# Optimization experiments

Measured on AMD Instinct MI355X. Metric: run time of the kernel, lower is better.

## Reference

```python
import jax, jax.numpy as jnp
import numpy as np

# dims: batch, seq, model, heads, head_dim, mlp, layers, vocab, window
B, S, D, H, DH, M, L, V, W = 2, 2048, 512, 8, 64, 2048, 6, 32000, 512
EPS = 1e-6
NEG = -1e9

def _sinusoidal(max_len, d):
    # LRA common_layers sinusoidal_init (min_scale=1, max_scale=1e4)
    pe = np.zeros((max_len, d), np.float32)
    position = np.arange(max_len)[:, None].astype(np.float32)
    scale_factor = -np.log(1e4) / (d // 2 - 1)
    div_term = np.exp(np.arange(d // 2).astype(np.float32) * scale_factor)
    pe[:, : d // 2] = np.sin(position * div_term)
    pe[:, d // 2 :] = np.cos(position * div_term)
    return jnp.asarray(pe)[None]  # [1, S, D]

POS_EMB = _sinusoidal(S, D)

def _ln(x, scale, bias):
    mu = jnp.mean(x, -1, keepdims=True)
    var = jnp.mean(jnp.square(x - mu), -1, keepdims=True)
    return (x - mu) * jax.lax.rsqrt(var + EPS) * scale + bias

def setup_inputs() -> dict:
    key = jax.random.key(0)
    ks = jax.random.split(key, 16)
    def n(k, shape, s=0.02):
        return jax.random.normal(k, shape, jnp.float32) * s
    return {
        "inputs": jax.random.randint(ks[0], (B, S), 0, V),
        "emb": n(ks[1], (V, D), 1.0),          # nn.Embed normal(stddev=1)
        "wq": n(ks[2], (L, D, H, DH)),
        "wk": n(ks[3], (L, D, H, DH)),
        "wv": n(ks[4], (L, D, H, DH)),
        "wo": n(ks[5], (L, H, DH, D)),
        "ln1_s": 1.0 + n(ks[6], (L, D)),
        "ln1_b": n(ks[7], (L, D)),
        "ln2_s": 1.0 + n(ks[8], (L, D)),
        "ln2_b": n(ks[9], (L, D)),
        "w1": n(ks[10], (L, D, M)),
        "b1": n(ks[11], (L, M), 1e-6),
        "w2": n(ks[12], (L, M, D)),
        "b2": n(ks[13], (L, D), 1e-6),
        "lnf_s": 1.0 + n(ks[14], (D,)),
        "lnf_b": n(ks[15], (D,)),
    }

def reference(inputs, emb, wq, wk, wv, wo, ln1_s, ln1_b, ln2_s, ln2_b,
              w1, b1, w2, b2, lnf_s, lnf_b):
    pad = inputs > 0                                  # [B,S] padding mask
    x = emb[inputs] + POS_EMB                         # embed + sinusoidal pos
    idx = jnp.arange(S)
    band = jnp.abs(idx[:, None] - idx[None, :]) <= (W // 2)  # sliding window
    mask = band[None, None] & pad[:, None, :, None] & pad[:, None, None, :]
    attn_bias = jnp.where(mask, 0.0, NEG)             # [B,1,S,S]
    scale = 1.0 / jnp.sqrt(jnp.float32(DH))
    for l in range(L):
        # --- Longformer self-attention (pre-LN) ---
        y = _ln(x, ln1_s[l], ln1_b[l])
        q = jnp.einsum('bsd,dhk->bshk', y, wq[l]) * scale
        k = jnp.einsum('bsd,dhk->bshk', y, wk[l])
        v = jnp.einsum('bsd,dhk->bshk', y, wv[l])
        logits = jnp.einsum('bqhk,bshk->bhqs', q, k) + attn_bias
        attn = jax.nn.softmax(logits, axis=-1)
        o = jnp.einsum('bhqs,bshk->bqhk', attn, v)
        x = x + jnp.einsum('bqhk,hkd->bqd', o, wo[l])
        # --- MLP block (pre-LN) ---
        y = _ln(x, ln2_s[l], ln2_b[l])
        h = jax.nn.gelu(jnp.einsum('bsd,dm->bsm', y, w1[l]) + b1[l])
        x = x + jnp.einsum('bsm,md->bsd', h, w2[l]) + b2[l]
    return _ln(x, lnf_s, lnf_b)                       # encoder_norm -> [B,S,D]
```

## Files before the change

### kernel.cpp

```cpp
#include <hip/hip_runtime.h>
#include <hip/hip_bf16.h>
#include <math.h>

#define B_    2
#define S_    2048
#define D_    512
#define H_    8
#define DH_   64
#define M_    2048
#define L_    6

typedef float f4v __attribute__((ext_vector_type(4)));
typedef short s8v __attribute__((ext_vector_type(8)));
typedef unsigned short u16;

#define GLOAD16(gp, lp) __builtin_amdgcn_global_load_lds( \
    (const __attribute__((address_space(1))) void*)(gp),  \
    (__attribute__((address_space(3))) void*)(lp), 16, 0, 0)

__device__ __forceinline__ unsigned pack2bf(float a, float b) {
    __hip_bfloat162 t;
    t.x = __float2bfloat16(a);
    t.y = __float2bfloat16(b);
    return *(unsigned*)&t;
}
__device__ __forceinline__ float bf2f(u16 u) {
    unsigned v = ((unsigned)u) << 16;
    return *(float*)&v;
}

__global__ __launch_bounds__(256) void embed_kernel(
    const int* __restrict__ tok, const float* __restrict__ emb,
    float* __restrict__ x, int* __restrict__ pad)
{
    int t = blockIdx.x;
    int s = t & (S_ - 1);
    int d = threadIdx.x;
    int tk = tok[t];
    if (d == 0) pad[t] = (tk > 0) ? 1 : 0;
    const float sf = -9.210340371976184f / 255.0f;
    float dt  = expf((float)d * sf);
    float ang = (float)s * dt;
    x[(size_t)t * D_ + d]       = emb[(size_t)tk * D_ + d]       + sinf(ang);
    x[(size_t)t * D_ + d + 256] = emb[(size_t)tk * D_ + d + 256] + cosf(ang);
}

template<bool OBF16>
__global__ __launch_bounds__(256) void ln_kernel(
    const float* __restrict__ xin, const float* __restrict__ sc,
    const float* __restrict__ bi, void* __restrict__ yout)
{
    int t = blockIdx.x;
    int d2 = threadIdx.x;
    float2 xv = *(const float2*)&xin[(size_t)t * D_ + 2 * d2];
    float ssum = xv.x + xv.y;
    float ssq  = xv.x * xv.x + xv.y * xv.y;
    #pragma unroll
    for (int m = 32; m; m >>= 1) {
        ssum += __shfl_xor(ssum, m);
        ssq  += __shfl_xor(ssq,  m);
    }
    __shared__ float smem[8];
    int wave = threadIdx.x >> 6, lane = threadIdx.x & 63;
    if (lane == 0) { smem[wave] = ssum; smem[4 + wave] = ssq; }
    __syncthreads();
    float tsum = smem[0] + smem[1] + smem[2] + smem[3];
    float tsq  = smem[4] + smem[5] + smem[6] + smem[7];
    float mu  = tsum * (1.0f / D_);
    float var = tsq * (1.0f / D_) - mu * mu;
    float r   = rsqrtf(var + 1e-6f);
    float2 sv = *(const float2*)&sc[2 * d2];
    float2 bv = *(const float2*)&bi[2 * d2];
    float ox = (xv.x - mu) * r * sv.x + bv.x;
    float oy = (xv.y - mu) * r * sv.y + bv.y;
    if (OBF16) {
        __hip_bfloat16* y = (__hip_bfloat16*)yout;
        __hip_bfloat162 p;
        p.x = __float2bfloat16(ox); p.y = __float2bfloat16(oy);
        *(__hip_bfloat162*)&y[(size_t)t * D_ + 2 * d2] = p;
    } else {
        float* y = (float*)yout;
        float2 ov; ov.x = ox; ov.y = oy;
        *(float2*)&y[(size_t)t * D_ + 2 * d2] = ov;
    }
}

__global__ __launch_bounds__(256) void transpose_cast(
    const float* __restrict__ wq, const float* __restrict__ wk,
    const float* __restrict__ wv, const float* __restrict__ wo,
    const float* __restrict__ w1, const float* __restrict__ w2,
    __hip_bfloat16* __restrict__ dst)
{
    __shared__ float tile[32][33];
    const int l = blockIdx.y;
    const int bx = blockIdx.x;
    const size_t lbase = (size_t)l * 3145728;
    const float* src; __hip_bfloat16* d; int K, N, kt, nt;
    float wscale = 1.0f;
    if (bx < 1024) {
        int m = bx >> 8, t = bx & 255;
        const float* s4 = (m == 0) ? wq : (m == 1) ? wk : (m == 2) ? wv : wo;
        if (m == 0) wscale = 0.125f;
        src = s4 + (size_t)l * 262144;
        d = dst + lbase + (size_t)m * 262144;
        K = 512; N = 512; kt = t >> 4; nt = t & 15;
    } else if (bx < 2048) {
        int t = bx - 1024;
        src = w1 + (size_t)l * 1048576;
        d = dst + lbase + 1048576;
        K = 512; N = 2048; kt = t >> 6; nt = t & 63;
    } else {
        int t = bx - 2048;
        src = w2 + (size_t)l * 1048576;
        d = dst + lbase + 2097152;
        K = 2048; N = 512; kt = t >> 4; nt = t & 15;
    }
    const int x = threadIdx.x & 31, y = threadIdx.x >> 5;
    const int kk0 = kt * 32, nn0 = nt * 32;
    #pragma unroll
    for (int p = 0; p < 4; ++p)
        tile[y + p * 8][x] = src[(size_t)(kk0 + y + p * 8) * N + nn0 + x];
    __syncthreads();
    #pragma unroll
    for (int p = 0; p < 4; ++p)
        d[(size_t)(nn0 + y + p * 8) * K + kk0 + x] =
            __float2bfloat16(tile[x][y + p * 8] * wscale);
}

__device__ __forceinline__ float gelu_tanh(float xx) {
    float u = fminf(fmaxf(xx, -10.f), 10.f);
    float t = 0.7978845608028654f * (u + 0.044715f * u * u * u);
    float e = __expf(2.f * t);
    float th = 1.f - 2.f * __builtin_amdgcn_rcpf(e + 1.f);
    return 0.5f * xx * (1.f + th);
}

template<bool OUT_BF16, int TAG>
__global__ __launch_bounds__(512) void gemm_sk(
    const __hip_bfloat16* __restrict__ A, const __hip_bfloat16* __restrict__ Wt,
    const float* __restrict__ bias, const float* __restrict__ resid,
    void* __restrict__ Cout, int K, int ldc, int ncol, int gelu)
{
    __shared__ __align__(16) char lds[73728];

    const int nwg = gridDim.x;
    const int cpx = nwg >> 3;
    const int bid = blockIdx.x;
    const int pos = (bid & 7) * cpx + (bid >> 3);
    const int row0 = (pos / ncol) * 128;
    const int col0 = (pos % ncol) * 64;

    const int tid = threadIdx.x, lane = tid & 63, w = tid >> 6;
    const int kg = w >> 2, wg = w & 3;
    const int wr = wg >> 1, wc = wg & 1;
    const int lq = lane & 15, g = lane >> 4;

    const int Kpart = K >> 1;
    const int nt = Kpart >> 5;
    const char* Ab = (const char*)A;
    const char* Bt = (const char*)Wt;
    const int ldsrow = lane >> 2;
    const int swzseg = (lane & 3) ^ ((lane >> 3) & 3);
    const int slot8  = (g ^ ((lq >> 1) & 3)) * 8;

    f4v acc[4][2] = {};

    auto STAGE = [&](int c, int t) {
        const int k0 = kg * Kpart + t * 32;
        char* dst = lds + (kg * 3 + c) * 12288;
        #pragma unroll
        for (int i2 = 0; i2 < 2; ++i2) {
            int seg = wg * 2 + i2;
            const char* gp = Ab + ((size_t)(row0 + seg * 16 + ldsrow) * K + k0) * 2 + swzseg * 16;
            GLOAD16(gp, dst + seg * 1024);
        }
        {
            const char* gp = Bt + ((size_t)(col0 + wg * 16 + ldsrow) * K + k0) * 2 + swzseg * 16;
            GLOAD16(gp, dst + 8192 + wg * 1024);
        }
    };

    STAGE(0, 0);
    STAGE(1, 1);
    STAGE(2, 2);

    for (int t = 0; t < nt; ++t) {
        if (t < nt - 2)      asm volatile("s_waitcnt vmcnt(6)" ::: "memory");
        else if (t < nt - 1) asm volatile("s_waitcnt vmcnt(3)" ::: "memory");
        else                 asm volatile("s_waitcnt vmcnt(0)" ::: "memory");
        __builtin_amdgcn_s_barrier();
        __builtin_amdgcn_sched_barrier(0);

        const unsigned short* Al = (const unsigned short*)(lds + (kg * 3 + t % 3) * 12288);
        const unsigned short* Bl = Al + 4096;
        s8v af[4], bfv[2];
        #pragma unroll
        for (int mi = 0; mi < 4; ++mi)
            af[mi] = *(const s8v*)&Al[(wr * 64 + mi * 16 + lq) * 32 + slot8];
        #pragma unroll
        for (int ni = 0; ni < 2; ++ni)
            bfv[ni] = *(const s8v*)&Bl[(wc * 32 + ni * 16 + lq) * 32 + slot8];

        __builtin_amdgcn_s_setprio(1);
        #pragma unroll
        for (int mi = 0; mi < 4; ++mi)
            #pragma unroll
            for (int ni = 0; ni < 2; ++ni)
                acc[mi][ni] = __builtin_amdgcn_mfma_f32_16x16x32_bf16(af[mi], bfv[ni], acc[mi][ni], 0, 0, 0);
        __builtin_amdgcn_s_setprio(0);

        asm volatile("s_waitcnt lgkmcnt(0)" ::: "memory");
        __builtin_amdgcn_s_barrier();
        __builtin_amdgcn_sched_barrier(0);
        if (t + 3 < nt) STAGE(t % 3, t + 3);
    }

    float* scr = (float*)lds;
    if (kg == 1) {
        #pragma unroll
        for (int mi = 0; mi < 4; ++mi)
            #pragma unroll
            for (int ni = 0; ni < 2; ++ni)
                *(f4v*)&scr[(((mi * 2 + ni) * 4 + wg) * 64 + lane) * 4] = acc[mi][ni];
    }
    __syncthreads();
    if (kg == 1) return;

    #pragma unroll
    for (int mi = 0; mi < 4; ++mi)
        #pragma unroll
        for (int ni = 0; ni < 2; ++ni)
            acc[mi][ni] += *(const f4v*)&scr[(((mi * 2 + ni) * 4 + wg) * 64 + lane) * 4];

    #pragma unroll
    for (int mi = 0; mi < 4; ++mi) {
        #pragma unroll
        for (int ni = 0; ni < 2; ++ni) {
            #pragma unroll
            for (int jj = 0; jj < 4; ++jj) {
                int rrow = row0 + wr * 64 + mi * 16 + g * 4 + jj;
                int ccol = col0 + wc * 32 + ni * 16 + lq;
                float vv = acc[mi][ni][jj];
                if (bias)  vv += bias[ccol];
                if (gelu)  vv = gelu_tanh(vv);
                if (resid) vv += resid[(size_t)rrow * ldc + ccol];
                if (OUT_BF16)
                    ((__hip_bfloat16*)Cout)[(size_t)rrow * ldc + ccol] = __float2bfloat16(vv);
                else
                    ((float*)Cout)[(size_t)rrow * ldc + ccol] = vv;
            }
        }
    }
}

template<bool OUT_BF16, int TAG>
__global__ __launch_bounds__(256) void gemm_sk64(
    const __hip_bfloat16* __restrict__ A, const __hip_bfloat16* __restrict__ Wt,
    const float* __restrict__ bias, const float* __restrict__ resid,
    void* __restrict__ Cout, int K, int ldc, int ncol, int gelu)
{
    __shared__ __align__(16) char lds[49152];

    const int nwg = gridDim.x;
    const int cpx = nwg >> 3;
    const int bid = blockIdx.x;
    const int pos = (bid & 7) * cpx + (bid >> 3);
    const int row0 = (pos / ncol) * 64;
    const int col0 = (pos % ncol) * 64;

    const int tid = threadIdx.x, lane = tid & 63, w = tid >> 6;
    const int kg = w >> 1, wg = w & 1;
    const int lq = lane & 15, g = lane >> 4;

    const int Kpart = K >> 1;
    const int nt = Kpart >> 5;
    const char* Ab = (const char*)A;
    const char* Bt = (const char*)Wt;
    const int ldsrow = lane >> 2;
    const int swzseg = (lane & 3) ^ ((lane >> 3) & 3);
    const int slot8  = (g ^ ((lq >> 1) & 3)) * 8;

    f4v acc[4][2] = {};

    auto STAGE = [&](int c, int t) {
        const int k0 = kg * Kpart + t * 32;
        char* dst = lds + (kg * 3 + c) * 8192;
        #pragma unroll
        for (int i2 = 0; i2 < 2; ++i2) {
            int seg = wg * 2 + i2;
            const char* gp = Ab + ((size_t)(row0 + seg * 16 + ldsrow) * K + k0) * 2 + swzseg * 16;
            GLOAD16(gp, dst + seg * 1024);
        }
        #pragma unroll
        for (int i2 = 0; i2 < 2; ++i2) {
            int seg = wg * 2 + i2;
            const char* gp = Bt + ((size_t)(col0 + seg * 16 + ldsrow) * K + k0) * 2 + swzseg * 16;
            GLOAD16(gp, dst + 4096 + seg * 1024);
        }
    };

    STAGE(0, 0);
    STAGE(1, 1);
    STAGE(2, 2);

    for (int t = 0; t < nt; ++t) {
        if (t < nt - 2)      asm volatile("s_waitcnt vmcnt(8)" ::: "memory");
        else if (t < nt - 1) asm volatile("s_waitcnt vmcnt(4)" ::: "memory");
        else                 asm volatile("s_waitcnt vmcnt(0)" ::: "memory");
        __builtin_amdgcn_s_barrier();
        __builtin_amdgcn_sched_barrier(0);

        const unsigned short* Al = (const unsigned short*)(lds + (kg * 3 + t % 3) * 8192);
        const unsigned short* Bl = Al + 2048;
        s8v af[4], bfv[2];
        #pragma unroll
        for (int mi = 0; mi < 4; ++mi)
            af[mi] = *(const s8v*)&Al[(mi * 16 + lq) * 32 + slot8];
        #pragma unroll
        for (int ni = 0; ni < 2; ++ni)
            bfv[ni] = *(const s8v*)&Bl[(wg * 32 + ni * 16 + lq) * 32 + slot8];

        __builtin_amdgcn_s_setprio(1);
        #pragma unroll
        for (int mi = 0; mi < 4; ++mi)
            #pragma unroll
            for (int ni = 0; ni < 2; ++ni)
                acc[mi][ni] = __builtin_amdgcn_mfma_f32_16x16x32_bf16(af[mi], bfv[ni], acc[mi][ni], 0, 0, 0);
        __builtin_amdgcn_s_setprio(0);

        asm volatile("s_waitcnt lgkmcnt(0)" ::: "memory");
        __builtin_amdgcn_s_barrier();
        __builtin_amdgcn_sched_barrier(0);
        if (t + 3 < nt) STAGE(t % 3, t + 3);
    }

    float* scr = (float*)lds;
    if (kg == 1) {
        #pragma unroll
        for (int mi = 0; mi < 4; ++mi)
            #pragma unroll
            for (int ni = 0; ni < 2; ++ni)
                *(f4v*)&scr[(((mi * 2 + ni) * 2 + wg) * 64 + lane) * 4] = acc[mi][ni];
    }
    __syncthreads();
    if (kg == 1) return;

    #pragma unroll
    for (int mi = 0; mi < 4; ++mi)
        #pragma unroll
        for (int ni = 0; ni < 2; ++ni)
            acc[mi][ni] += *(const f4v*)&scr[(((mi * 2 + ni) * 2 + wg) * 64 + lane) * 4];

    #pragma unroll
    for (int mi = 0; mi < 4; ++mi) {
        #pragma unroll
        for (int ni = 0; ni < 2; ++ni) {
            #pragma unroll
            for (int jj = 0; jj < 4; ++jj) {
                int rrow = row0 + mi * 16 + g * 4 + jj;
                int ccol = col0 + wg * 32 + ni * 16 + lq;
                float vv = acc[mi][ni][jj];
                if (bias)  vv += bias[ccol];
                if (gelu)  vv = gelu_tanh(vv);
                if (resid) vv += resid[(size_t)rrow * ldc + ccol];
                if (OUT_BF16)
                    ((__hip_bfloat16*)Cout)[(size_t)rrow * ldc + ccol] = __float2bfloat16(vv);
                else
                    ((float*)Cout)[(size_t)rrow * ldc + ccol] = vv;
            }
        }
    }
}

__global__ __launch_bounds__(512) void attn_mfma_kernel(
    const u16* __restrict__ qkv, const int* __restrict__ pad,
    __hip_bfloat16* __restrict__ o)
{
    __shared__ __align__(16) unsigned short Klds[2][64 * 64];
    __shared__ __align__(16) unsigned short Vt[2][64 * 64];
    __shared__ float padfa[640];

    const int qt = blockIdx.x, bh = blockIdx.y;
    const int h = bh & 7, b = bh >> 3;
    const int q0 = qt * 128;
    const int tid = threadIdx.x, w = tid >> 6, lane = tid & 63;
    const int lq = lane & 15, g = lane >> 4;
    const int wq0 = q0 + w * 16;
    const size_t base = (size_t)b * S_ * 1536 + h * 64;

    for (int j = tid; j < 640; j += 512) {
        int krow = q0 - 256 + j;
        padfa[j] = (krow >= 0 && krow < S_ && pad[b * S_ + krow] != 0) ? 1.f : 0.f;
    }

    s8v qf[2];
    {
        const u16* qr = qkv + base + (size_t)(wq0 + lq) * 1536;
        #pragma unroll
        for (int ks = 0; ks < 2; ++ks)
            qf[ks] = *(const s8v*)&qr[ks * 32 + g * 8];
    }

    float lsum = 0.f;
    f4v oacc[4] = {};
    const int oblane = 256 + 4 * g - wq0 - lq;

    const int ki = tid >> 3, kss = tid & 7;
    const int vd = tid & 63, vkb = tid >> 6;
    s8v kreg;
    u16 vreg0, vreg1, vreg2, vreg3, vreg4, vreg5, vreg6, vreg7;

    auto LOAD_REGS = [&](int c) {
        const int kc = q0 - 256 + c * 64;
        {
            int krow = kc + ki;
            int kcl = krow < 0 ? 0 : (krow >= S_ ? S_ - 1 : krow);
            kreg = *(const s8v*)&qkv[base + 512 + (size_t)kcl * 1536 + kss * 8];
        }
        {
            int kr0 = kc + vkb * 8;
            const u16* vp = qkv + base + 1024 + vd;
            int c0 = kr0+0 < 0 ? 0 : (kr0+0 >= S_ ? S_-1 : kr0+0);
            int c1 = kr0+1 < 0 ? 0 : (kr0+1 >= S_ ? S_-1 : kr0+1);
            int c2 = kr0+2 < 0 ? 0 : (kr0+2 >= S_ ? S_-1 : kr0+2);
            int c3 = kr0+3 < 0 ? 0 : (kr0+3 >= S_ ? S_-1 : kr0+3);
            int c4 = kr0+4 < 0 ? 0 : (kr0+4 >= S_ ? S_-1 : kr0+4);
            int c5 = kr0+5 < 0 ? 0 : (kr0+5 >= S_ ? S_-1 : kr0+5);
            int c6 = kr0+6 < 0 ? 0 : (kr0+6 >= S_ ? S_-1 : kr0+6);
            int c7 = kr0+7 < 0 ? 0 : (kr0+7 >= S_ ? S_-1 : kr0+7);
            vreg0 = vp[(size_t)c0 * 1536]; vreg1 = vp[(size_t)c1 * 1536];
            vreg2 = vp[(size_t)c2 * 1536]; vreg3 = vp[(size_t)c3 * 1536];
            vreg4 = vp[(size_t)c4 * 1536]; vreg5 = vp[(size_t)c5 * 1536];
            vreg6 = vp[(size_t)c6 * 1536]; vreg7 = vp[(size_t)c7 * 1536];
        }
    };
    auto WRITE_LDS = [&](int buf) {
        *(s8v*)&Klds[buf][ki * 64 + ((kss ^ (ki & 7)) * 8)] = kreg;
        union { s8v s; u16 u[8]; } vv;
        vv.u[0] = vreg0; vv.u[1] = vreg1; vv.u[2] = vreg2; vv.u[3] = vreg3;
        vv.u[4] = vreg4; vv.u[5] = vreg5; vv.u[6] = vreg6; vv.u[7] = vreg7;
        *(s8v*)&Vt[buf][vd * 64 + ((vkb ^ (vd & 7)) * 8)] = vv.s;
    };

    LOAD_REGS(0);
    WRITE_LDS(0);
    LOAD_REGS(1);

    #pragma unroll 1
    for (int c = 0; c < 10; ++c) {
        asm volatile("s_waitcnt lgkmcnt(0)" ::: "memory");
        __builtin_amdgcn_s_barrier();
        __builtin_amdgcn_sched_barrier(0);
        const int kc = q0 - 256 + c * 64;
        const int buf = c & 1;

        #pragma unroll
        for (int sub = 0; sub < 2; ++sub) {
            const int kc2 = kc + sub * 32;
            if (kc2 + 31 < wq0 - 256 || kc2 > wq0 + 271) continue;

            f4v st[2] = {};
            __builtin_amdgcn_s_setprio(1);
            #pragma unroll
            for (int tt = 0; tt < 2; ++tt) {
                #pragma unroll
                for (int ks = 0; ks < 2; ++ks) {
                    const int row = sub * 32 + tt * 16 + lq;
                    const s8v af = *(const s8v*)&Klds[buf][row * 64 + (((ks * 4 + g) ^ (row & 7)) * 8)];
                    st[tt] = __builtin_amdgcn_mfma_f32_16x16x32_bf16(af, qf[ks], st[tt], 0, 0, 0);
                }
            }
            __builtin_amdgcn_s_setprio(0);

            float psum = 0.f;
            unsigned wpk[2][2];
            #pragma unroll
            for (int tt = 0; tt < 2; ++tt) {
                float pr[4];
                #pragma unroll
                for (int r = 0; r < 4; ++r) {
                    const int off = kc2 + 16 * tt + r + oblane;
                    float e = __expf(fminf(st[tt][r], 60.f)) *
                              padfa[c * 64 + sub * 32 + 16 * tt + 4 * g + r];
                    pr[r] = ((unsigned)off <= 512u) ? e : 0.f;
                    psum += pr[r];
                }
                wpk[tt][0] = pack2bf(pr[0], pr[1]);
                wpk[tt][1] = pack2bf(pr[2], pr[3]);
            }
            psum += __shfl_xor(psum, 16);
            psum += __shfl_xor(psum, 32);
            lsum += psum;

            const int srcA = (((2 * g) & 3) * 16 + lq) << 2;
            const int srcB = (((2 * g + 1) & 3) * 16 + lq) << 2;
            const bool hi = (g >= 2);
            union { s8v s; int u[4]; } pa;
            {
                int a0 = __builtin_amdgcn_ds_bpermute(srcA, (int)wpk[0][0]);
                int a1 = __builtin_amdgcn_ds_bpermute(srcA, (int)wpk[1][0]);
                pa.u[0] = hi ? a1 : a0;
                int b0 = __builtin_amdgcn_ds_bpermute(srcA, (int)wpk[0][1]);
                int b1 = __builtin_amdgcn_ds_bpermute(srcA, (int)wpk[1][1]);
                pa.u[1] = hi ? b1 : b0;
                int c0 = __builtin_amdgcn_ds_bpermute(srcB, (int)wpk[0][0]);
                int c1 = __builtin_amdgcn_ds_bpermute(srcB, (int)wpk[1][0]);
                pa.u[2] = hi ? c1 : c0;
                int d0 = __builtin_amdgcn_ds_bpermute(srcB, (int)wpk[0][1]);
                int d1 = __builtin_amdgcn_ds_bpermute(srcB, (int)wpk[1][1]);
                pa.u[3] = hi ? d1 : d0;
            }

            __builtin_amdgcn_s_setprio(1);
            #pragma unroll
            for (int dt = 0; dt < 4; ++dt) {
                const int row = dt * 16 + lq;
                const s8v vf = *(const s8v*)&Vt[buf][row * 64 + (((sub * 4 + g) ^ (row & 7)) * 8)];
                oacc[dt] = __builtin_amdgcn_mfma_f32_16x16x32_bf16(pa.s, vf, oacc[dt], 0, 0, 0);
            }
            __builtin_amdgcn_s_setprio(0);
        }

        if (c + 1 < 10) WRITE_LDS((c + 1) & 1);
        if (c + 2 < 10) LOAD_REGS(c + 2);
    }

    float inv = 1.0f / lsum;
    #pragma unroll
    for (int r = 0; r < 4; ++r) {
        int iv = __builtin_amdgcn_ds_bpermute((4 * g + r) << 2, __float_as_int(inv));
        float invq = __int_as_float(iv);
        const int qq = wq0 + 4 * g + r;
        __hip_bfloat16* orow = o + ((size_t)b * S_ + qq) * 512 + h * 64;
        #pragma unroll
        for (int dt = 0; dt < 4; ++dt)
            orow[dt * 16 + lq] = __float2bfloat16(oacc[dt][r] * invq);
    }

    {
        int padq = pad[b * S_ + wq0 + lq];
        unsigned long long bal = __ballot(g == 0 && padq == 0);
        if (bal) {
            #pragma unroll 1
            for (int r = 0; r < 16; ++r) {
                if (!((bal >> r) & 1ull)) continue;
                const int qq = wq0 + r;
                const float qd = bf2f(qkv[base + (size_t)qq * 1536 + lane]);
                float ls = 0.f, av = 0.f;
                #pragma unroll 1
                for (int s = 0; s < S_; ++s) {
                    float xp = qd * bf2f(qkv[base + 512 + (size_t)s * 1536 + lane]);
                    #pragma unroll
                    for (int m = 32; m; m >>= 1) xp += __shfl_xor(xp, m);
                    float p = __expf(fminf(xp, 60.f));
                    ls += p;
                    av += p * bf2f(qkv[base + 1024 + (size_t)s * 1536 + lane]);
                }
                o[((size_t)b * S_ + qq) * 512 + h * 64 + lane] = __float2bfloat16(av / ls);
            }
        }
    }
}

extern "C" void kernel_launch(void* const* d_in, const int* in_sizes, int n_in,
                              void* d_out, int out_size, void* d_ws, size_t ws_size,
                              hipStream_t stream)
{
    const int*   tok   = (const int*)  d_in[0];
    const float* emb   = (const float*)d_in[1];
    const float* wq    = (const float*)d_in[2];
    const float* wk    = (const float*)d_in[3];
    const float* wv    = (const float*)d_in[4];
    const float* wo    = (const float*)d_in[5];
    const float* ln1_s = (const float*)d_in[6];
    const float* ln1_b = (const float*)d_in[7];
    const float* ln2_s = (const float*)d_in[8];
    const float* ln2_b = (const float*)d_in[9];
    const float* w1    = (const float*)d_in[10];
    const float* b1    = (const float*)d_in[11];
    const float* w2    = (const float*)d_in[12];
    const float* b2    = (const float*)d_in[13];
    const float* lnf_s = (const float*)d_in[14];
    const float* lnf_b = (const float*)d_in[15];
    float* out = (float*)d_out;

    char* ws = (char*)d_ws;
    float*          x     = (float*)(ws + 0);
    __hip_bfloat16* ybf   = (__hip_bfloat16*)(ws + 8388608);
    __hip_bfloat16* qkvbf = (__hip_bfloat16*)(ws + 12582912);
    __hip_bfloat16* ob    = (__hip_bfloat16*)(ws + 37748736);
    __hip_bfloat16* hb    = (__hip_bfloat16*)(ws + 41943040);
    int*            pad   = (int*)(ws + 58720256);
    __hip_bfloat16* wT    = (__hip_bfloat16*)(ws + 58736640);

    const int NT = B_ * S_;

    transpose_cast<<<dim3(3072, L_), 256, 0, stream>>>(wq, wk, wv, wo, w1, w2, wT);
    embed_kernel<<<NT, 256, 0, stream>>>(tok, emb, x, pad);

    for (int l = 0; l < L_; ++l) {
        __hip_bfloat16* wTl = wT + (size_t)l * 3145728;
        ln_kernel<true><<<NT, 256, 0, stream>>>(x, ln1_s + l * D_, ln1_b + l * D_, (void*)ybf);
        gemm_sk<true, 0><<<768, 512, 0, stream>>>(ybf, wTl, nullptr, nullptr,
                                                  (void*)qkvbf, 512, 1536, 24, 0);
        attn_mfma_kernel<<<dim3(16, 16), 512, 0, stream>>>((const u16*)qkvbf, pad, ob);
        gemm_sk64<false, 1><<<512, 256, 0, stream>>>(ob, wTl + 786432, nullptr, x,
                                                     (void*)x, 512, 512, 8, 0);
        ln_kernel<true><<<NT, 256, 0, stream>>>(x, ln2_s + l * D_, ln2_b + l * D_, (void*)ybf);
        gemm_sk<true, 2><<<1024, 512, 0, stream>>>(ybf, wTl + 1048576, b1 + l * M_, nullptr,
                                                   (void*)hb, 512, 2048, 32, 1);
        gemm_sk64<false, 3><<<512, 256, 0, stream>>>(hb, wTl + 2097152, b2 + l * D_, x,
                                                     (void*)x, 2048, 512, 8, 0);
    }
    ln_kernel<false><<<NT, 256, 0, stream>>>(x, lnf_s, lnf_b, (void*)out);
}
```

Before: 779.2 us.

## Enlarge split-K output-projection GEMM tiles to 128x64 with 64-wide K steps

Replaces the 64x64 split-K GEMM used for the attention output and MLP down projections with a 128x64-tile, 512-thread version that stages 64-wide K slices into a larger triple-buffered LDS area using an XOR swizzle. Each wave now issues two MFMA K sub-steps per barrier, so there are half as many barrier/wait iterations, and each B tile is reused across more rows. The cost is 144KB of LDS per block and half the grid (256 blocks), which lowers occupancy and may leave some compute units idle on a 256-CU part.

```diff
diff --git a/kernel.cpp b/kernel.cpp
--- a/kernel.cpp
+++ b/kernel.cpp
@@ -254,48 +254,49 @@
 }
 
 template<bool OUT_BF16, int TAG>
-__global__ __launch_bounds__(256) void gemm_sk64(
+__global__ __launch_bounds__(512) void gemm_bk64(
     const __hip_bfloat16* __restrict__ A, const __hip_bfloat16* __restrict__ Wt,
     const float* __restrict__ bias, const float* __restrict__ resid,
     void* __restrict__ Cout, int K, int ldc, int ncol, int gelu)
 {
-    __shared__ __align__(16) char lds[49152];
+    __shared__ __align__(16) char lds[147456];
 
     const int nwg = gridDim.x;
     const int cpx = nwg >> 3;
     const int bid = blockIdx.x;
     const int pos = (bid & 7) * cpx + (bid >> 3);
-    const int row0 = (pos / ncol) * 64;
+    const int row0 = (pos / ncol) * 128;
     const int col0 = (pos % ncol) * 64;
 
     const int tid = threadIdx.x, lane = tid & 63, w = tid >> 6;
-    const int kg = w >> 1, wg = w & 1;
+    const int kg = w >> 2, wg = w & 3;
+    const int wr = wg >> 1, wc = wg & 1;
     const int lq = lane & 15, g = lane >> 4;
 
     const int Kpart = K >> 1;
-    const int nt = Kpart >> 5;
+    const int nt = Kpart >> 6;
     const char* Ab = (const char*)A;
     const char* Bt = (const char*)Wt;
-    const int ldsrow = lane >> 2;
-    const int swzseg = (lane & 3) ^ ((lane >> 3) & 3);
-    const int slot8  = (g ^ ((lq >> 1) & 3)) * 8;
+    const int srow8  = lane >> 3;
+    const int schunk = lane & 7;
+    const int gchunk = schunk ^ srow8;
 
     f4v acc[4][2] = {};
 
     auto STAGE = [&](int c, int t) {
-        const int k0 = kg * Kpart + t * 32;
-        char* dst = lds + (kg * 3 + c) * 8192;
+        const int k0 = kg * Kpart + t * 64;
+        char* dst = lds + (kg * 3 + c) * 24576;
+        #pragma unroll
+        for (int i2 = 0; i2 < 4; ++i2) {
+            int seg = wg * 4 + i2;
+            const char* gp = Ab + ((size_t)(row0 + seg * 8 + srow8) * K + k0) * 2 + gchunk * 16;
+            GLOAD16(gp, dst + seg * 1024);
+        }
         #pragma unroll
         for (int i2 = 0; i2 < 2; ++i2) {
             int seg = wg * 2 + i2;
-            const char* gp = Ab + ((size_t)(row0 + seg * 16 + ldsrow) * K + k0) * 2 + swzseg * 16;
-            GLOAD16(gp, dst + seg * 1024);
-        }
-        #pragma unroll
-        for (int i2 = 0; i2 < 2; ++i2) {
-            int seg = wg * 2 + i2;
-            const char* gp = Bt + ((size_t)(col0 + seg * 16 + ldsrow) * K + k0) * 2 + swzseg * 16;
-            GLOAD16(gp, dst + 4096 + seg * 1024);
+            const char* gp = Bt + ((size_t)(col0 + seg * 8 + srow8) * K + k0) * 2 + gchunk * 16;
+            GLOAD16(gp, dst + 16384 + seg * 1024);
         }
     };
 
@@ -304,28 +305,37 @@
     STAGE(2, 2);
 
     for (int t = 0; t < nt; ++t) {
-        if (t < nt - 2)      asm volatile("s_waitcnt vmcnt(8)" ::: "memory");
-        else if (t < nt - 1) asm volatile("s_waitcnt vmcnt(4)" ::: "memory");
+        if (t < nt - 2)      asm volatile("s_waitcnt vmcnt(12)" ::: "memory");
+        else if (t < nt - 1) asm volatile("s_waitcnt vmcnt(6)" ::: "memory");
         else                 asm volatile("s_waitcnt vmcnt(0)" ::: "memory");
         __builtin_amdgcn_s_barrier();
         __builtin_amdgcn_sched_barrier(0);
 
-        const unsigned short* Al = (const unsigned short*)(lds + (kg * 3 + t % 3) * 8192);
-        const unsigned short* Bl = Al + 2048;
-        s8v af[4], bfv[2];
-        #pragma unroll
-        for (int mi = 0; mi < 4; ++mi)
-            af[mi] = *(const s8v*)&Al[(mi * 16 + lq) * 32 + slot8];
-        #pragma unroll
-        for (int ni = 0; ni < 2; ++ni)
-            bfv[ni] = *(const s8v*)&Bl[(wg * 32 + ni * 16 + lq) * 32 + slot8];
+        const unsigned short* Al = (const unsigned short*)(lds + (kg * 3 + t % 3) * 24576);
+        const unsigned short* Bl = Al + 8192;
+        s8v af[4][2], bfv[2][2];
+        #pragma unroll
+        for (int ks = 0; ks < 2; ++ks) {
+            #pragma unroll
+            for (int mi = 0; mi < 4; ++mi) {
+                const int r = wr * 64 + mi * 16 + lq;
+                af[mi][ks] = *(const s8v*)&Al[r * 64 + (((ks * 4 + g) ^ (r & 7)) * 8)];
+            }
+            #pragma unroll
+            for (int ni = 0; ni < 2; ++ni) {
+                const int r = wc * 32 + ni * 16 + lq;
+                bfv[ni][ks] = *(const s8v*)&Bl[r * 64 + (((ks * 4 + g) ^ (r & 7)) * 8)];
+            }
+        }
 
         __builtin_amdgcn_s_setprio(1);
         #pragma unroll
-        for (int mi = 0; mi < 4; ++mi)
-            #pragma unroll
-            for (int ni = 0; ni < 2; ++ni)
-                acc[mi][ni] = __builtin_amdgcn_mfma_f32_16x16x32_bf16(af[mi], bfv[ni], acc[mi][ni], 0, 0, 0);
+        for (int ks = 0; ks < 2; ++ks)
+            #pragma unroll
+            for (int mi = 0; mi < 4; ++mi)
+                #pragma unroll
+                for (int ni = 0; ni < 2; ++ni)
+                    acc[mi][ni] = __builtin_amdgcn_mfma_f32_16x16x32_bf16(af[mi][ks], bfv[ni][ks], acc[mi][ni], 0, 0, 0);
         __builtin_amdgcn_s_setprio(0);
 
         asm volatile("s_waitcnt lgkmcnt(0)" ::: "memory");
@@ -340,7 +350,7 @@
         for (int mi = 0; mi < 4; ++mi)
             #pragma unroll
             for (int ni = 0; ni < 2; ++ni)
-                *(f4v*)&scr[(((mi * 2 + ni) * 2 + wg) * 64 + lane) * 4] = acc[mi][ni];
+                *(f4v*)&scr[(((mi * 2 + ni) * 4 + wg) * 64 + lane) * 4] = acc[mi][ni];
     }
     __syncthreads();
     if (kg == 1) return;
@@ -349,7 +359,7 @@
     for (int mi = 0; mi < 4; ++mi)
         #pragma unroll
         for (int ni = 0; ni < 2; ++ni)
-            acc[mi][ni] += *(const f4v*)&scr[(((mi * 2 + ni) * 2 + wg) * 64 + lane) * 4];
+            acc[mi][ni] += *(const f4v*)&scr[(((mi * 2 + ni) * 4 + wg) * 64 + lane) * 4];
 
     #pragma unroll
     for (int mi = 0; mi < 4; ++mi) {
@@ -357,8 +367,8 @@
         for (int ni = 0; ni < 2; ++ni) {
             #pragma unroll
             for (int jj = 0; jj < 4; ++jj) {
-                int rrow = row0 + mi * 16 + g * 4 + jj;
-                int ccol = col0 + wg * 32 + ni * 16 + lq;
+                int rrow = row0 + wr * 64 + mi * 16 + g * 4 + jj;
+                int ccol = col0 + wc * 32 + ni * 16 + lq;
                 float vv = acc[mi][ni][jj];
                 if (bias)  vv += bias[ccol];
                 if (gelu)  vv = gelu_tanh(vv);
@@ -604,12 +614,12 @@
         gemm_sk<true, 0><<<768, 512, 0, stream>>>(ybf, wTl, nullptr, nullptr,
                                                   (void*)qkvbf, 512, 1536, 24, 0);
         attn_mfma_kernel<<<dim3(16, 16), 512, 0, stream>>>((const u16*)qkvbf, pad, ob);
-        gemm_sk64<false, 1><<<512, 256, 0, stream>>>(ob, wTl + 786432, nullptr, x,
+        gemm_bk64<false, 1><<<256, 512, 0, stream>>>(ob, wTl + 786432, nullptr, x,
                                                      (void*)x, 512, 512, 8, 0);
         ln_kernel<true><<<NT, 256, 0, stream>>>(x, ln2_s + l * D_, ln2_b + l * D_, (void*)ybf);
         gemm_sk<true, 2><<<1024, 512, 0, stream>>>(ybf, wTl + 1048576, b1 + l * M_, nullptr,
                                                    (void*)hb, 512, 2048, 32, 1);
-        gemm_sk64<false, 3><<<512, 256, 0, stream>>>(hb, wTl + 2097152, b2 + l * D_, x,
+        gemm_bk64<false, 3><<<256, 512, 0, stream>>>(hb, wTl + 2097152, b2 + l * D_, x,
                                                      (void*)x, 2048, 512, 8, 0);
     }
     ln_kernel<false><<<NT, 256, 0, stream>>>(x, lnf_s, lnf_b, (void*)out);
```

New measurement: 731.8 us. -6.1%, faster.
